# Kernel tuning notes

Hardware: AMD Instinct MI355X
Metric: run time of the kernel (lower is better)

The kernel has to match this reference:

```python
import jax, jax.numpy as jnp
import numpy as np

N, C_IN, T, V = 128, 64, 64, 25
K = 3           # num_subsets
C_OUT = 192
MID = 64        # int((1/K) * C_OUT)
EPS = 1e-5


def conv1x1(x, W, b):
    # x: (n,c,t,v), W: (o,c), b: (o,)  -> (n,o,t,v)
    return jnp.einsum('nctv,oc->notv', x, W) + b[None, :, None, None]


def bn_eval(x, p):
    # p: (4,C) rows = gamma, beta, running_mean, running_var
    g, b, m, v = p[0], p[1], p[2], p[3]
    scale = (g * jax.lax.rsqrt(v + EPS))[None, :, None, None]
    return x * scale + (b - m * g * jax.lax.rsqrt(v + EPS))[None, :, None, None]


def _bn_params(key, c):
    kg, kb, km, kv = jax.random.split(key, 4)
    return jnp.stack([
        1.0 + 0.1 * jax.random.normal(kg, (c,), jnp.float32),
        0.1 * jax.random.normal(kb, (c,), jnp.float32),
        0.1 * jax.random.normal(km, (c,), jnp.float32),
        0.5 + jax.random.uniform(kv, (c,), jnp.float32),
    ])


def setup_inputs() -> dict:
    key = jax.random.key(0)
    ks = jax.random.split(key, 20)
    rn = lambda k, shape, s=1.0: s * jax.random.normal(k, shape, jnp.float32)
    return {
        'x': rn(ks[0], (N, C_IN, T, V)),
        'A': rn(ks[1], (K, V, V), 0.1),
        'alpha': rn(ks[2], (K,), 0.1),
        'beta': rn(ks[3], (K,), 0.1),
        'W_pre': rn(ks[4], (MID * K, C_IN), 0.05), 'b_pre': rn(ks[5], (MID * K,), 0.05),
        'bn_pre': _bn_params(ks[6], MID * K),
        'W1': rn(ks[7], (MID * K, C_IN), 0.05), 'b1': rn(ks[8], (MID * K,), 0.05),
        'W2': rn(ks[9], (MID * K, C_IN), 0.05), 'b2': rn(ks[10], (MID * K,), 0.05),
        'W_post': rn(ks[11], (C_OUT, MID * K), 0.05), 'b_post': rn(ks[12], (C_OUT,), 0.05),
        'bn_post': _bn_params(ks[13], C_OUT),
        'W_down': rn(ks[14], (C_OUT, C_IN), 0.05), 'b_down': rn(ks[15], (C_OUT,), 0.05),
        'bn_down': _bn_params(ks[16], C_OUT),
    }


def reference(x, A, alpha, beta, W_pre, b_pre, bn_pre, W1, b1, W2, b2,
              W_post, b_post, bn_post, W_down, b_down, bn_down):
    n = x.shape[0]
    # residual branch (in_channels != out_channels -> conv + BN)
    res = bn_eval(conv1x1(x, W_down, b_down), bn_down)
    # pre: conv1x1 -> BN -> ReLU, reshaped to (n,k,mid,t,v)
    pre_x = jax.nn.relu(bn_eval(conv1x1(x, W_pre, b_pre), bn_pre)).reshape(n, K, MID, T, V)
    # ctr/ada both active and neither 'NA' -> temporal mean
    tmp = x.mean(axis=2, keepdims=True)                      # (n,c,1,v)
    x1 = conv1x1(tmp, W1, b1).reshape(n, K, MID, 1, V)       # (n,k,mid,1,v)
    x2 = conv1x1(tmp, W2, b2).reshape(n, K, MID, 1, V)
    # ctr branch: tanh(pairwise diff) * alpha[0], added to static A
    diff = jnp.tanh(x1[..., :, None] - x2[..., None, :]) * alpha[0]   # (n,k,mid,1,v,v)
    Adyn = diff + A[None, :, None, None]                              # broadcast (1,k,1,1,v,v)
    # ada branch: softmax(x1^T x2) over axis -2, scaled by beta[0]
    ada = jnp.einsum('nkctv,nkctw->nktvw', x1, x2)[:, :, None]        # (n,k,1,1,v,v)
    ada = jax.nn.softmax(ada, axis=-2) * beta[0]
    Adyn = Adyn + ada                                                 # (n,k,mid,1,v,v)
    # A.shape[3] == 1 path: squeeze t-dim, channel-wise adjacency
    Adyn = Adyn[:, :, :, 0]                                           # (n,k,mid,v,v)
    y = jnp.einsum('nkctv,nkcvw->nkctw', pre_x, Adyn).reshape(n, K * MID, T, V)
    y = conv1x1(y, W_post, b_post)
    return jax.nn.relu(bn_eval(y, bn_post) + res)
```

## Files before the change

kernel.cpp:

```cpp
#include <hip/hip_runtime.h>
#include <hip/hip_bf16.h>

typedef __hip_bfloat16 bf16;
typedef __attribute__((ext_vector_type(8))) short s16x8;
typedef __attribute__((ext_vector_type(4))) float f32x4;

constexpr int cN = 128, cC = 64, cT = 64, cV = 25, cK = 3, cMID = 64, cKM = 192, cTV = 1600;
constexpr float cEPS = 1e-5f;

__device__ float g_tmp[cN * cC * cV];
__device__ ushort g_adF[(size_t)cN * cKM * 1024];
__device__ ushort g_WpreF[2 * 12 * 512];
__device__ ushort g_WcatF[8 * 12 * 512];
__device__ float g_bpre [cKM];
__device__ float g_cterm[cKM];

__device__ __forceinline__ ushort f2bu(float v){ return __builtin_bit_cast(ushort, __float2bfloat16(v)); }

__global__ __launch_bounds__(256) void k_fold(
    const float* __restrict__ Wpre, const float* __restrict__ bpre,
    const float* __restrict__ bnpre,
    const float* __restrict__ Wpost, const float* __restrict__ bpost,
    const float* __restrict__ bnpost,
    const float* __restrict__ Wdown, const float* __restrict__ bdown,
    const float* __restrict__ bndown){
  __shared__ float sPre[24], sPost[24], sDown[24];
  int ob = blockIdx.x * 24;
  int tid = threadIdx.x;
  if (tid < 24){
    int o = ob + tid;
    float sp = bnpre[o] * rsqrtf(bnpre[3*cKM+o] + cEPS);
    sPre[tid] = sp;
    g_bpre[o] = bpre[o]*sp + bnpre[cKM+o] - bnpre[2*cKM+o]*sp;
    float sP = bnpost[o] * rsqrtf(bnpost[3*cKM+o] + cEPS);
    float sD = bndown[o] * rsqrtf(bndown[3*cKM+o] + cEPS);
    sPost[tid] = sP; sDown[tid] = sD;
    g_cterm[o] = bpost[o]*sP + bnpost[cKM+o] - bnpost[2*cKM+o]*sP
               + bdown[o]*sD + bndown[cKM+o] - bndown[2*cKM+o]*sD;
  }
  __syncthreads();
  for (int i = tid; i < 24*cC; i += 256){
    int ol = i >> 6, k = i & 63;
    int o = ob + ol;
    int step = k >> 5, g = (k >> 3) & 3, j = k & 7;
    int dst = ((step*12 + (o>>4)) << 9) + (((g<<4) | (o&15)) << 3) + j;
    g_WpreF[dst] = f2bu(Wpre[o*cC + k] * sPre[ol]);
  }
  for (int i = tid; i < 24*256; i += 256){
    int ol = i >> 8, k = i & 255;
    int o = ob + ol;
    float w = (k < cKM) ? Wpost[o*cKM + k] * sPost[ol]
                        : Wdown[o*cC + (k - cKM)] * sDown[ol];
    int step = k >> 5, g = (k >> 3) & 3, j = k & 7;
    int dst = ((step*12 + (o>>4)) << 9) + (((g<<4) | (o&15)) << 3) + j;
    g_WcatF[dst] = f2bu(w);
  }
}

__global__ __launch_bounds__(256) void gm_tmp(const float* __restrict__ x){
  __shared__ float xs[4 * cTV];
  int n = blockIdx.x >> 4, cg = blockIdx.x & 15;
  int tid = threadIdx.x;
  const float* xp = x + ((size_t)n*cC + cg*4)*cTV;
  for (int i = tid; i < 4*cTV; i += 256) xs[i] = xp[i];
  __syncthreads();
  if (tid < 100){
    int c = tid / 25, v = tid - c*25;
    float s = 0.f;
    #pragma unroll
    for (int t = 0; t < cT; ++t) s += xs[c*cTV + t*cV + v];
    g_tmp[(n*cC + cg*4 + c)*cV + v] = s * (1.f/cT);
  }
}

__global__ __launch_bounds__(256) void gm_prep(
    const float* __restrict__ W1, const float* __restrict__ b1,
    const float* __restrict__ W2, const float* __restrict__ b2,
    const float* __restrict__ A,  const float* __restrict__ alpha,
    const float* __restrict__ beta){
  __shared__ float tl [cC*cV];
  __shared__ float x1l[cMID*cV];
  __shared__ float x2l[cMID*cV];
  __shared__ float adal[cV*cV];
  __shared__ float Al [cV*cV];
  int bid = blockIdx.x; int n = bid / 3, kg = bid % 3;
  int tid = threadIdx.x;
  for (int i = tid; i < cC*cV; i += 256) tl[i] = g_tmp[n*cC*cV + i];
  for (int i = tid; i < cV*cV; i += 256) Al[i] = A[kg*625 + i];
  __syncthreads();
  for (int idx = tid; idx < cMID*cV; idx += 256){
    int ch = idx / cV, v = idx % cV;
    int o = kg*cMID + ch;
    float s1 = b1[o], s2 = b2[o];
    const float* w1p = W1 + o*cC;
    const float* w2p = W2 + o*cC;
    #pragma unroll 8
    for (int c = 0; c < cC; ++c){
      float t = tl[c*cV + v];
      s1 += w1p[c]*t; s2 += w2p[c]*t;
    }
    x1l[idx] = s1; x2l[idx] = s2;
  }
  __syncthreads();
  for (int idx = tid; idx < cV*cV; idx += 256){
    int v = idx / cV, w = idx % cV;
    float s = 0.f;
    #pragma unroll 8
    for (int c = 0; c < cMID; ++c) s += x1l[c*cV + v] * x2l[c*cV + w];
    adal[idx] = s;
  }
  __syncthreads();
  float b0 = beta[0];
  if (tid < cV){
    int w = tid;
    float m = -1e30f;
    for (int v = 0; v < cV; ++v) m = fmaxf(m, adal[v*cV + w]);
    float s = 0.f;
    for (int v = 0; v < cV; ++v) s += __expf(adal[v*cV + w] - m);
    float inv = b0 / s;
    for (int v = 0; v < cV; ++v) adal[v*cV + w] = __expf(adal[v*cV + w] - m) * inv;
  }
  __syncthreads();
  float a0 = alpha[0];
  ushort* dst = g_adF + ((size_t)n*cKM + kg*cMID) * 1024;
  #pragma unroll 1
  for (int e0 = 0; e0 < 65536; e0 += 512){
    int e = e0 + tid*2;
    int ch = e >> 10, rem = e & 1023;
    int nf = rem >> 9, r2 = rem & 511;
    int li = r2 >> 3, j0 = r2 & 7;
    int v0 = 8*(li >> 4) + j0, w = 16*nf + (li & 15);
    float f0 = 0.f, f1 = 0.f;
    if (w < cV){
      float xw = x2l[ch*cV + w];
      float shared = Al[0];
      (void)shared;
      if (v0 < cV){
        float e2 = __expf(2.f*(x1l[ch*cV + v0] - xw));
        f0 = __fdividef(e2-1.f, e2+1.f)*a0 + Al[v0*cV + w] + adal[v0*cV + w];
      }
      if (v0 + 1 < cV){
        float e2 = __expf(2.f*(x1l[ch*cV + v0+1] - xw));
        f1 = __fdividef(e2-1.f, e2+1.f)*a0 + Al[(v0+1)*cV + w] + adal[(v0+1)*cV + w];
      }
    }
    uint pk = (uint)f2bu(f0) | ((uint)f2bu(f1) << 16);
    *(uint*)&dst[e] = pk;
  }
}

__global__ __launch_bounds__(512, 4) void gm_fused(const float* __restrict__ x,
                                                   float* __restrict__ outf){
  __shared__ ushort Zl[32 * 128 * 8];
  __shared__ ushort Pt[64 * 128];
  int bid = (int)(blockIdx.x & 7) * 256 + ((int)blockIdx.x >> 3);
  int n = bid >> 4, ttile = bid & 15;
  int t0 = ttile * 4;
  int tid = threadIdx.x;
  int wv = tid >> 6, lane = tid & 63, g = lane >> 4, l15 = lane & 15;
  int mfh = wv >> 1;
  int nfh = wv & 1;

  #pragma unroll
  for (int s0 = 0; s0 < 1024; s0 += 512){
    int s = s0 + tid;
    int oct = s >> 7, col = s & 127;
    int t = col >> 5, v = col & 31;
    ushort u[8];
    if (v < cV){
      const float* xp = x + ((size_t)n*cC + oct*8)*cTV + (t0 + t)*cV + v;
      #pragma unroll
      for (int j = 0; j < 8; ++j) u[j] = f2bu(xp[(size_t)j*cTV]);
    } else {
      #pragma unroll
      for (int j = 0; j < 8; ++j) u[j] = 0;
    }
    *(uint4*)&Zl[((24 + oct)*128 + col)*8] = *(const uint4*)u;
  }

  #pragma unroll 1
  for (int kg = 0; kg < 3; ++kg){
    __syncthreads();
    s16x8 bva0[8], bva1[8];
    #pragma unroll
    for (int cc = 0; cc < 8; ++cc){
      const ushort* bp = g_adF + ((size_t)n*cKM + kg*64 + wv*8 + cc)*1024;
      bva0[cc] = *(const s16x8*)(bp + lane*8);
      bva1[cc] = *(const s16x8*)(bp + 512 + lane*8);
    }
    f32x4 a1[4];
    #pragma unroll
    for (int nn = 0; nn < 4; ++nn) a1[nn] = (f32x4){0.f,0.f,0.f,0.f};
    #pragma unroll
    for (int ks = 0; ks < 2; ++ks){
      s16x8 av = *(const s16x8*)(g_WpreF + ((ks*12 + kg*4 + mfh) << 9) + lane*8);
      #pragma unroll
      for (int nn = 0; nn < 4; ++nn){
        int col = 16*(nfh*4 + nn) + l15;
        s16x8 bv = *(const s16x8*)&Zl[((24 + ks*4 + g)*128 + col)*8];
        a1[nn] = __builtin_amdgcn_mfma_f32_16x16x32_bf16(av, bv, a1[nn], 0, 0, 0);
      }
    }
    #pragma unroll
    for (int nn = 0; nn < 4; ++nn){
      int col = 16*(nfh*4 + nn) + l15;
      int t = col >> 5, v = col & 31;
      #pragma unroll
      for (int q = 0; q < 4; ++q){
        int o = 16*mfh + 4*g + q;
        float val = (v < cV) ? fmaxf(a1[nn][q] + g_bpre[kg*64 + o], 0.f) : 0.f;
        int slot = ((v>>3) ^ (o>>2)) & 3;
        Pt[o*128 + slot*32 + t*8 + (v & 7)] = f2bu(val);
      }
    }
    __syncthreads();
    #pragma unroll
    for (int cc = 0; cc < 8; ++cc){
      int chl = wv*8 + cc;
      s16x8 av;
      if (l15 < 4){
        int slot = (g ^ (chl>>2)) & 3;
        av = *(const s16x8*)&Pt[chl*128 + slot*32 + l15*8];
      } else av = (s16x8){0,0,0,0,0,0,0,0};
      f32x4 d0 = __builtin_amdgcn_mfma_f32_16x16x32_bf16(av, bva0[cc], (f32x4){0.f,0.f,0.f,0.f}, 0, 0, 0);
      f32x4 d1 = __builtin_amdgcn_mfma_f32_16x16x32_bf16(av, bva1[cc], (f32x4){0.f,0.f,0.f,0.f}, 0, 0, 0);
      if (g == 0){
        #pragma unroll
        for (int q = 0; q < 4; ++q){
          Zl[((kg*8 + (chl>>3))*128 + q*32 + l15)*8 + (chl&7)] = f2bu(d0[q]);
          Zl[((kg*8 + (chl>>3))*128 + q*32 + 16 + l15)*8 + (chl&7)] = f2bu(d1[q]);
        }
      }
    }
  }
  __syncthreads();
  f32x4 a3[3][4];
  #pragma unroll
  for (int mm = 0; mm < 3; ++mm)
    #pragma unroll
    for (int nn = 0; nn < 4; ++nn) a3[mm][nn] = (f32x4){0.f,0.f,0.f,0.f};
  s16x8 avc[3], avn[3];
  #pragma unroll
  for (int mm = 0; mm < 3; ++mm)
    avc[mm] = *(const s16x8*)(g_WcatF + ((0*12 + mfh*3 + mm) << 9) + lane*8);
  #pragma unroll 1
  for (int ks = 0; ks < 8; ++ks){
    if (ks < 7){
      #pragma unroll
      for (int mm = 0; mm < 3; ++mm)
        avn[mm] = *(const s16x8*)(g_WcatF + (((ks+1)*12 + mfh*3 + mm) << 9) + lane*8);
    }
    s16x8 bv[4];
    #pragma unroll
    for (int nn = 0; nn < 4; ++nn){
      int col = 16*(nfh*4 + nn) + l15;
      bv[nn] = *(const s16x8*)&Zl[((ks*4 + g)*128 + col)*8];
    }
    #pragma unroll
    for (int mm = 0; mm < 3; ++mm)
      #pragma unroll
      for (int nn = 0; nn < 4; ++nn)
        a3[mm][nn] = __builtin_amdgcn_mfma_f32_16x16x32_bf16(avc[mm], bv[nn], a3[mm][nn], 0, 0, 0);
    #pragma unroll
    for (int mm = 0; mm < 3; ++mm) avc[mm] = avn[mm];
  }
  #pragma unroll
  for (int mm = 0; mm < 3; ++mm){
    #pragma unroll
    for (int q = 0; q < 4; ++q){
      int o = 48*mfh + 16*mm + 4*g + q;
      float ct = g_cterm[o];
      #pragma unroll
      for (int nn = 0; nn < 4; ++nn){
        int col = 16*(nfh*4 + nn) + l15;
        int t = col >> 5, v = col & 31;
        if (v < cV)
          outf[((size_t)n*cKM + o)*cTV + (t0 + t)*cV + v] = fmaxf(a3[mm][nn][q] + ct, 0.f);
      }
    }
  }
}

extern "C" void kernel_launch(void* const* d_in, const int* in_sizes, int n_in,
                              void* d_out, int out_size, void* d_ws, size_t ws_size,
                              hipStream_t stream){
  (void)in_sizes; (void)n_in; (void)out_size; (void)d_ws; (void)ws_size;
  const float* x      = (const float*)d_in[0];
  const float* A      = (const float*)d_in[1];
  const float* alpha  = (const float*)d_in[2];
  const float* beta   = (const float*)d_in[3];
  const float* W_pre  = (const float*)d_in[4];
  const float* b_pre  = (const float*)d_in[5];
  const float* bn_pre = (const float*)d_in[6];
  const float* W1     = (const float*)d_in[7];
  const float* b1     = (const float*)d_in[8];
  const float* W2     = (const float*)d_in[9];
  const float* b2     = (const float*)d_in[10];
  const float* W_post = (const float*)d_in[11];
  const float* b_post = (const float*)d_in[12];
  const float* bn_post= (const float*)d_in[13];
  const float* W_down = (const float*)d_in[14];
  const float* b_down = (const float*)d_in[15];
  const float* bn_down= (const float*)d_in[16];
  float* out = (float*)d_out;

  k_fold  <<<8,        256, 0, stream>>>(W_pre, b_pre, bn_pre,
                                         W_post, b_post, bn_post,
                                         W_down, b_down, bn_down);
  gm_tmp  <<<cN * 16,  256, 0, stream>>>(x);
  gm_prep <<<cN * 3,   256, 0, stream>>>(W1, b1, W2, b2, A, alpha, beta);
  gm_fused<<<cN * 16,  512, 0, stream>>>(x, out);
}
```

Measured before the change: 191.4 us.

## Merge weight folding into temporal-mean kernel and restructure adjacency prep

Merges the BN/weight folding kernel into the temporal-mean kernel, so the first 8 blocks do the folding after the mean and one launch is removed. The adjacency prep kernel now uses 512 threads and stages W1/W2 in padded shared memory. Each thread computes four vertices of the x1/x2 projection, reusing each weight load. The static A and softmax terms are pre-summed once, and each thread keeps its (v,w) position fixed across channels, which removes per-element index math and two shared loads per output. The cost is more shared memory per block, which may lower occupancy of the prep kernel.

```diff
diff --git a/kernel.cpp b/kernel.cpp
--- a/kernel.cpp
+++ b/kernel.cpp
@@ -17,16 +17,32 @@
 
 __device__ __forceinline__ ushort f2bu(float v){ return __builtin_bit_cast(ushort, __float2bfloat16(v)); }
 
-__global__ __launch_bounds__(256) void k_fold(
+__global__ __launch_bounds__(256) void gm_tmp(const float* __restrict__ x,
     const float* __restrict__ Wpre, const float* __restrict__ bpre,
     const float* __restrict__ bnpre,
     const float* __restrict__ Wpost, const float* __restrict__ bpost,
     const float* __restrict__ bnpost,
     const float* __restrict__ Wdown, const float* __restrict__ bdown,
     const float* __restrict__ bndown){
-  __shared__ float sPre[24], sPost[24], sDown[24];
+  __shared__ float xs[4 * cTV];
+  int n = blockIdx.x >> 4, cg = blockIdx.x & 15;
+  int tid = threadIdx.x;
+  const float* xp = x + ((size_t)n*cC + cg*4)*cTV;
+  for (int i = tid; i < 4*cTV; i += 256) xs[i] = xp[i];
+  __syncthreads();
+  if (tid < 100){
+    int c = tid / 25, v = tid - c*25;
+    float s = 0.f;
+    #pragma unroll
+    for (int t = 0; t < cT; ++t) s += xs[c*cTV + t*cV + v];
+    g_tmp[(n*cC + cg*4 + c)*cV + v] = s * (1.f/cT);
+  }
+  if (blockIdx.x >= 8) return;
+  __syncthreads();
+  float* sPre  = xs;
+  float* sPost = xs + 32;
+  float* sDown = xs + 64;
   int ob = blockIdx.x * 24;
-  int tid = threadIdx.x;
   if (tid < 24){
     int o = ob + tid;
     float sp = bnpre[o] * rsqrtf(bnpre[3*cKM+o] + cEPS);
@@ -57,52 +73,53 @@
   }
 }
 
-__global__ __launch_bounds__(256) void gm_tmp(const float* __restrict__ x){
-  __shared__ float xs[4 * cTV];
-  int n = blockIdx.x >> 4, cg = blockIdx.x & 15;
-  int tid = threadIdx.x;
-  const float* xp = x + ((size_t)n*cC + cg*4)*cTV;
-  for (int i = tid; i < 4*cTV; i += 256) xs[i] = xp[i];
-  __syncthreads();
-  if (tid < 100){
-    int c = tid / 25, v = tid - c*25;
-    float s = 0.f;
-    #pragma unroll
-    for (int t = 0; t < cT; ++t) s += xs[c*cTV + t*cV + v];
-    g_tmp[(n*cC + cg*4 + c)*cV + v] = s * (1.f/cT);
-  }
-}
-
-__global__ __launch_bounds__(256) void gm_prep(
+__global__ __launch_bounds__(512) void gm_prep(
     const float* __restrict__ W1, const float* __restrict__ b1,
     const float* __restrict__ W2, const float* __restrict__ b2,
     const float* __restrict__ A,  const float* __restrict__ alpha,
     const float* __restrict__ beta){
-  __shared__ float tl [cC*cV];
+  __shared__ float tl [cC*cV + 32];
+  __shared__ float w1l[cMID*65];
+  __shared__ float w2l[cMID*65];
   __shared__ float x1l[cMID*cV];
   __shared__ float x2l[cMID*cV];
+  __shared__ float Al [cV*cV];
   __shared__ float adal[cV*cV];
-  __shared__ float Al [cV*cV];
   int bid = blockIdx.x; int n = bid / 3, kg = bid % 3;
   int tid = threadIdx.x;
-  for (int i = tid; i < cC*cV; i += 256) tl[i] = g_tmp[n*cC*cV + i];
-  for (int i = tid; i < cV*cV; i += 256) Al[i] = A[kg*625 + i];
-  __syncthreads();
-  for (int idx = tid; idx < cMID*cV; idx += 256){
-    int ch = idx / cV, v = idx % cV;
+  for (int i = tid; i < cC*cV; i += 512) tl[i] = g_tmp[n*cC*cV + i];
+  if (tid < 32) tl[cC*cV + tid] = 0.f;
+  for (int i = tid; i < cV*cV; i += 512) Al[i] = A[kg*625 + i];
+  for (int i = tid; i < cMID*cC; i += 512){
+    int ch = i >> 6, c = i & 63;
+    w1l[ch*65 + c] = W1[(kg*cMID + ch)*cC + c];
+    w2l[ch*65 + c] = W2[(kg*cMID + ch)*cC + c];
+  }
+  __syncthreads();
+  {
+    int ch = tid >> 3, iv = tid & 7;
     int o = kg*cMID + ch;
-    float s1 = b1[o], s2 = b2[o];
-    const float* w1p = W1 + o*cC;
-    const float* w2p = W2 + o*cC;
+    float bb1 = b1[o], bb2 = b2[o];
+    float s1[4] = {bb1, bb1, bb1, bb1};
+    float s2[4] = {bb2, bb2, bb2, bb2};
     #pragma unroll 8
     for (int c = 0; c < cC; ++c){
-      float t = tl[c*cV + v];
-      s1 += w1p[c]*t; s2 += w2p[c]*t;
-    }
-    x1l[idx] = s1; x2l[idx] = s2;
-  }
-  __syncthreads();
-  for (int idx = tid; idx < cV*cV; idx += 256){
+      float w1c = w1l[ch*65 + c], w2c = w2l[ch*65 + c];
+      #pragma unroll
+      for (int k = 0; k < 4; ++k){
+        float t = tl[c*cV + iv + 8*k];
+        s1[k] += w1c * t;
+        s2[k] += w2c * t;
+      }
+    }
+    #pragma unroll
+    for (int k = 0; k < 4; ++k){
+      int v = iv + 8*k;
+      if (v < cV){ x1l[ch*cV + v] = s1[k]; x2l[ch*cV + v] = s2[k]; }
+    }
+  }
+  __syncthreads();
+  for (int idx = tid; idx < cV*cV; idx += 512){
     int v = idx / cV, w = idx % cV;
     float s = 0.f;
     #pragma unroll 8
@@ -121,31 +138,33 @@
     for (int v = 0; v < cV; ++v) adal[v*cV + w] = __expf(adal[v*cV + w] - m) * inv;
   }
   __syncthreads();
+  for (int i = tid; i < cV*cV; i += 512) Al[i] += adal[i];
+  __syncthreads();
   float a0 = alpha[0];
-  ushort* dst = g_adF + ((size_t)n*cKM + kg*cMID) * 1024;
-  #pragma unroll 1
-  for (int e0 = 0; e0 < 65536; e0 += 512){
-    int e = e0 + tid*2;
-    int ch = e >> 10, rem = e & 1023;
-    int nf = rem >> 9, r2 = rem & 511;
-    int li = r2 >> 3, j0 = r2 & 7;
-    int v0 = 8*(li >> 4) + j0, w = 16*nf + (li & 15);
+  int rem = tid * 2;
+  int nf = rem >> 9, r2 = rem & 511;
+  int li = r2 >> 3, j0 = r2 & 7;
+  int v0 = 8*(li >> 4) + j0, w = 16*nf + (li & 15);
+  bool wok = (w < cV);
+  bool v0ok = wok && (v0 < cV), v1ok = wok && (v0 + 1 < cV);
+  float AW0 = v0ok ? Al[v0*cV + w] : 0.f;
+  float AW1 = v1ok ? Al[(v0+1)*cV + w] : 0.f;
+  uint* dst = (uint*)(g_adF + ((size_t)n*cKM + kg*cMID)*1024 + rem);
+  #pragma unroll 4
+  for (int ch = 0; ch < cMID; ++ch){
     float f0 = 0.f, f1 = 0.f;
-    if (w < cV){
+    if (wok){
       float xw = x2l[ch*cV + w];
-      float shared = Al[0];
-      (void)shared;
-      if (v0 < cV){
+      if (v0ok){
         float e2 = __expf(2.f*(x1l[ch*cV + v0] - xw));
-        f0 = __fdividef(e2-1.f, e2+1.f)*a0 + Al[v0*cV + w] + adal[v0*cV + w];
-      }
-      if (v0 + 1 < cV){
-        float e2 = __expf(2.f*(x1l[ch*cV + v0+1] - xw));
-        f1 = __fdividef(e2-1.f, e2+1.f)*a0 + Al[(v0+1)*cV + w] + adal[(v0+1)*cV + w];
-      }
-    }
-    uint pk = (uint)f2bu(f0) | ((uint)f2bu(f1) << 16);
-    *(uint*)&dst[e] = pk;
+        f0 = __fdividef(e2 - 1.f, e2 + 1.f)*a0 + AW0;
+      }
+      if (v1ok){
+        float e2 = __expf(2.f*(x1l[ch*cV + v0 + 1] - xw));
+        f1 = __fdividef(e2 - 1.f, e2 + 1.f)*a0 + AW1;
+      }
+    }
+    dst[(size_t)ch * 512] = (uint)f2bu(f0) | ((uint)f2bu(f1) << 16);
   }
 }
 
@@ -304,10 +323,9 @@
   const float* bn_down= (const float*)d_in[16];
   float* out = (float*)d_out;
 
-  k_fold  <<<8,        256, 0, stream>>>(W_pre, b_pre, bn_pre,
+  gm_tmp  <<<cN * 16,  256, 0, stream>>>(x, W_pre, b_pre, bn_pre,
                                          W_post, b_post, bn_post,
                                          W_down, b_down, bn_down);
-  gm_tmp  <<<cN * 16,  256, 0, stream>>>(x);
-  gm_prep <<<cN * 3,   256, 0, stream>>>(W1, b1, W2, b2, A, alpha, beta);
+  gm_prep <<<cN * 3,   512, 0, stream>>>(W1, b1, W2, b2, A, alpha, beta);
   gm_fused<<<cN * 16,  512, 0, stream>>>(x, out);
 }
```

After: 163.9 us. 1.17x faster.
